# Performance work log

Measured on AMD Instinct MI355X. Metric: run time of the kernel, lower is better.

Reference implementation:

```python
import jax, jax.numpy as jnp
import numpy as np

N_NODES = 100000
N_EDGES = 500000
E_HID = 64
IN_DIM = 192  # r_hidden + 2*t_hidden
NEG_SLOPE = 0.01


def setup_inputs() -> dict:
    key = jax.random.key(0)
    ks = jax.random.split(key, 16)
    s_in = 1.0 / np.sqrt(IN_DIM)
    s_e = 1.0 / np.sqrt(E_HID)
    inp = {
        "x_e": jax.random.normal(ks[0], (N_NODES, E_HID), dtype=jnp.float32),
        "x_r": jax.random.normal(ks[1], (N_EDGES, IN_DIM), dtype=jnp.float32),
        "edge_index": jax.random.randint(ks[2], (2, N_EDGES), 0, N_NODES, dtype=jnp.int64),
        "rel_size": jnp.arange(N_EDGES, dtype=jnp.int64),
        "Wr": jax.random.uniform(ks[3], (E_HID, IN_DIM), jnp.float32, -s_in, s_in),
        "br": jax.random.uniform(ks[4], (E_HID,), jnp.float32, -s_in, s_in),
        "Wr1": jax.random.uniform(ks[5], (E_HID, IN_DIM), jnp.float32, -s_in, s_in),
        "br1": jax.random.uniform(ks[6], (E_HID,), jnp.float32, -s_in, s_in),
        "Wr2": jax.random.uniform(ks[7], (E_HID, IN_DIM), jnp.float32, -s_in, s_in),
        "br2": jax.random.uniform(ks[8], (E_HID,), jnp.float32, -s_in, s_in),
        "ah": jax.random.uniform(ks[9], (E_HID,), jnp.float32, -s_e, s_e),
        "ah1": jax.random.uniform(ks[10], (E_HID,), jnp.float32, -s_e, s_e),
        "at": jax.random.uniform(ks[11], (E_HID,), jnp.float32, -s_e, s_e),
        "ar1": jax.random.uniform(ks[12], (E_HID,), jnp.float32, -s_e, s_e),
        "ar2": jax.random.uniform(ks[13], (E_HID,), jnp.float32, -s_e, s_e),
        "ar3": jax.random.uniform(ks[14], (E_HID,), jnp.float32, -s_e, s_e),
    }
    return inp


def _gat_block(x_e, x_r, idx, rel_size, W, b, a_node, a_rel, num_nodes):
    # e_r = w_r(x_r): [E, e_hid]
    e_r = x_r @ W.T + b
    # attention logits per edge: a_node . x_e[idx] + a_rel . e_r
    logits = x_e[idx] @ a_node + e_r @ a_rel  # [E]
    lr = jnp.where(logits > 0, logits, NEG_SLOPE * logits)  # leaky_relu
    # segment softmax over destination segments (idx)
    m = jax.ops.segment_max(lr, idx, num_segments=num_nodes)
    ex = jnp.exp(lr - m[idx])
    s = jax.ops.segment_sum(ex, idx, num_segments=num_nodes)
    alpha = ex / (s[idx] + 1e-16)
    # spmm: out[n] = sum_{e: idx[e]==n} alpha[e] * e_r[rel_size[e]]
    agg = jax.ops.segment_sum(alpha[:, None] * e_r[rel_size], idx, num_segments=num_nodes)
    return x_e + jax.nn.relu(agg)


def reference(x_e, x_r, edge_index, rel_size, Wr, br, Wr1, br1, Wr2, br2,
              ah, ah1, at, ar1, ar2, ar3):
    n = x_e.shape[0]
    h, t = edge_index[0], edge_index[1]
    x_e = _gat_block(x_e, x_r, h, rel_size, Wr, br, ah, ar1, n)
    x_e = _gat_block(x_e, x_r, t, rel_size, Wr1, br1, at, ar2, n)
    x_e = _gat_block(x_e, x_r, h, rel_size, Wr2, br2, ah1, ar3, n)
    return x_e
```

## Files before the change

kernel.cpp:

```cpp
#include <hip/hip_runtime.h>
#include <hip/hip_bf16.h>

typedef __attribute__((ext_vector_type(8))) short short8;
typedef __attribute__((ext_vector_type(4))) float f32x4;

#define DEV __device__ __forceinline__

#define BARRIER() do { asm volatile("s_waitcnt lgkmcnt(0)" ::: "memory"); \
                       __builtin_amdgcn_s_barrier(); \
                       __builtin_amdgcn_sched_barrier(0); } while (0)

DEV unsigned short f2bf(float f) {
    unsigned u = __float_as_uint(f);
    u += 0x7FFFu + ((u >> 16) & 1u);
    return (unsigned short)(u >> 16);
}
DEV float bf2f(unsigned short h) { return __uint_as_float(((unsigned)h) << 16); }
DEV unsigned pk2(float lo, float hi) {
    float2 f; f.x = lo; f.y = hi;
    __hip_bfloat162 h = __float22bfloat162_rn(f);
    unsigned r; __builtin_memcpy(&r, &h, 4);
    return r;
}
union S8 { short8 s; unsigned u[4]; };

__global__ __launch_bounds__(256) void wconv_k(
    const float* __restrict__ W0, const float* __restrict__ W1,
    const float* __restrict__ W2, unsigned short* __restrict__ wbf)
{
    const int i = blockIdx.x * 256 + threadIdx.x;
    if (i >= 3 * 64 * 192) return;
    const int m = i / (64 * 192), r = i % (64 * 192);
    const float* W = (m == 0) ? W0 : ((m == 1) ? W1 : W2);
    wbf[i] = f2bf(W[r]);
}

__global__ __launch_bounds__(512, 2) void gemm_k(
    const float* __restrict__ xr, const unsigned short* __restrict__ wbf,
    const float* __restrict__ b0, const float* __restrict__ b1, const float* __restrict__ b2,
    const float* __restrict__ a0, const float* __restrict__ a1, const float* __restrict__ a2,
    unsigned short* __restrict__ er,
    float* __restrict__ ed0, float* __restrict__ ed1, float* __restrict__ ed2,
    int E, int ntiles, int K)
{
    __shared__ __align__(16) unsigned short ShBuf[192 * 192];
    unsigned short* Ws = ShBuf;
    unsigned short* As = ShBuf;
    float (*red)[64] = (float (*)[64])(ShBuf + 64 * 192);

    const int t = threadIdx.x;
    const int w = t >> 6, l = t & 63, l15 = l & 15, lg = l >> 4;
    const int cgrp = w & 3, rh = w >> 2;
    const int srow = t >> 3, sq = t & 7;

#pragma unroll
    for (int j = 0; j < 9; ++j) {
        const int c = j * 512 + t;
        const int gc = c / 24, pos = c - gc * 24;
        const short8 v = *(const short8*)(wbf + (size_t)gc * 192 + pos * 8);
        const unsigned byte = (unsigned)(gc * 384 + pos * 16);
        *(short8*)((char*)Ws + (byte ^ ((gc & 7) << 4))) = v;
    }
    BARRIER();
    short8 bfr[3][6];
#pragma unroll
    for (int i = 0; i < 3; ++i) {
        const int gc = (cgrp * 3 + i) * 16 + l15;
#pragma unroll
        for (int ks = 0; ks < 6; ++ks) {
            const unsigned byte = (unsigned)(gc * 384 + ks * 64 + lg * 16);
            bfr[i][ks] = *(const short8*)((const char*)Ws + (byte ^ ((gc & 7) << 4)));
        }
    }

    const int G = gridDim.x;
    float4 nv[6];
    if (blockIdx.x < ntiles) {
        const long e = (long)blockIdx.x * 64 + srow;
        const bool ok = e < E;
        const float* sp = xr + e * (long)K + sq * 24;
#pragma unroll
        for (int r = 0; r < 6; ++r)
            nv[r] = ok ? *(const float4*)(sp + r * 4) : make_float4(0.f, 0.f, 0.f, 0.f);
    }

    for (int tile = blockIdx.x; tile < ntiles; tile += G) {
        const long e0 = (long)tile * 64;
        BARRIER();
        {
            const unsigned swz = (unsigned)((srow & 7) << 4);
            S8 o0, o1, o2;
            o0.u[0] = pk2(nv[0].x, nv[0].y); o0.u[1] = pk2(nv[0].z, nv[0].w);
            o0.u[2] = pk2(nv[1].x, nv[1].y); o0.u[3] = pk2(nv[1].z, nv[1].w);
            o1.u[0] = pk2(nv[2].x, nv[2].y); o1.u[1] = pk2(nv[2].z, nv[2].w);
            o1.u[2] = pk2(nv[3].x, nv[3].y); o1.u[3] = pk2(nv[3].z, nv[3].w);
            o2.u[0] = pk2(nv[4].x, nv[4].y); o2.u[1] = pk2(nv[4].z, nv[4].w);
            o2.u[2] = pk2(nv[5].x, nv[5].y); o2.u[3] = pk2(nv[5].z, nv[5].w);
            const unsigned byte0 = (unsigned)(srow * 384 + sq * 48);
            *(short8*)((char*)As + ((byte0 +  0) ^ swz)) = o0.s;
            *(short8*)((char*)As + ((byte0 + 16) ^ swz)) = o1.s;
            *(short8*)((char*)As + ((byte0 + 32) ^ swz)) = o2.s;
        }
        {
            const int nxt = tile + G;
            if (nxt < ntiles) {
                const long e = (long)nxt * 64 + srow;
                const bool ok = e < E;
                const float* sp = xr + e * (long)K + sq * 24;
#pragma unroll
                for (int r = 0; r < 6; ++r)
                    nv[r] = ok ? *(const float4*)(sp + r * 4)
                               : make_float4(0.f, 0.f, 0.f, 0.f);
            }
        }
        BARRIER();
        f32x4 acc[2][3];
#pragma unroll
        for (int rt = 0; rt < 2; ++rt)
#pragma unroll
            for (int i = 0; i < 3; ++i) acc[rt][i] = (f32x4)(0.f);
#pragma unroll
        for (int ks = 0; ks < 6; ++ks) {
            short8 af[2];
#pragma unroll
            for (int rt = 0; rt < 2; ++rt) {
                const int row = rh * 32 + rt * 16 + l15;
                const unsigned byte = (unsigned)(row * 384 + ks * 64 + lg * 16);
                af[rt] = *(const short8*)((const char*)As + (byte ^ ((row & 7) << 4)));
            }
#pragma unroll
            for (int i = 0; i < 3; ++i)
#pragma unroll
                for (int rt = 0; rt < 2; ++rt)
                    acc[rt][i] = __builtin_amdgcn_mfma_f32_16x16x32_bf16(bfr[i][ks], af[rt], acc[rt][i], 0, 0, 0);
        }
#pragma unroll
        for (int i = 0; i < 3; ++i) {
            const int ct = cgrp * 3 + i, m = ct >> 2;
            const int cb_ = ((ct & 3) << 4) + (lg << 2);
            const float* bp = (m == 0) ? b0 : ((m == 1) ? b1 : b2);
            const float* ap = (m == 0) ? a0 : ((m == 1) ? a1 : a2);
            const float4 bb = *(const float4*)(bp + cb_);
            const float4 aa = *(const float4*)(ap + cb_);
            const int fb = ct * 16 + (lg << 2);
#pragma unroll
            for (int rt = 0; rt < 2; ++rt) {
                const int edge = rh * 32 + rt * 16 + l15;
                const long ee = e0 + edge;
                const float v0 = acc[rt][i][0] + bb.x;
                const float v1 = acc[rt][i][1] + bb.y;
                const float v2 = acc[rt][i][2] + bb.z;
                const float v3 = acc[rt][i][3] + bb.w;
                if (ee < E) {
                    uint2 pkv;
                    pkv.x = pk2(v0, v1);
                    pkv.y = pk2(v2, v3);
                    *(uint2*)(er + (size_t)ee * 192 + fb) = pkv;
                }
                float pd = v0 * aa.x + v1 * aa.y + v2 * aa.z + v3 * aa.w;
                pd += __shfl_xor(pd, 16);
                pd += __shfl_xor(pd, 32);
                if (lg == 0) red[ct][edge] = pd;
            }
        }
        BARRIER();
        if (t < 64) {
            const long ee = e0 + t;
            if (ee < E) {
                float s0 = 0.f, s1 = 0.f, s2 = 0.f;
#pragma unroll
                for (int q = 0; q < 4; ++q) {
                    s0 += red[q][t]; s1 += red[4 + q][t]; s2 += red[8 + q][t];
                }
                ed0[ee] = s0; ed1[ee] = s1; ed2[ee] = s2;
            }
        }
    }
}

__global__ __launch_bounds__(256) void count2_k(const int* __restrict__ h,
                                                const int* __restrict__ tt,
                                                int* __restrict__ deg, int E, int N)
{
    const int e = blockIdx.x * 256 + threadIdx.x;
    if (e >= E) return;
    atomicAdd(&deg[h[e]], 1);
    atomicAdd(&deg[N + tt[e]], 1);
}

__global__ __launch_bounds__(256) void scan1_k(const int* __restrict__ deg,
                                               int* __restrict__ incl,
                                               int* __restrict__ bsum, int M)
{
    __shared__ int buf[256];
    const int tid = threadIdx.x;
    const int n = blockIdx.x * 256 + tid;
    buf[tid] = (n < M) ? deg[n] : 0;
    __syncthreads();
    for (int d = 1; d < 256; d <<= 1) {
        int v = (tid >= d) ? buf[tid - d] : 0;
        __syncthreads();
        buf[tid] += v;
        __syncthreads();
    }
    if (n < M) incl[n] = buf[tid];
    if (tid == 255) bsum[blockIdx.x] = buf[255];
}

__global__ __launch_bounds__(256) void scan2_k(int* __restrict__ bsum, int nb)
{
    __shared__ int wsum[4];
    const int tid = threadIdx.x, l = tid & 63, wv = tid >> 6;
    int base = 0;
    for (int start = 0; start < nb; start += 1024) {
        const int i0 = start + tid * 4;
        int v0 = 0, v1 = 0, v2 = 0, v3 = 0;
        if (i0 < nb)     v0 = bsum[i0];
        if (i0 + 1 < nb) v1 = bsum[i0 + 1];
        if (i0 + 2 < nb) v2 = bsum[i0 + 2];
        if (i0 + 3 < nb) v3 = bsum[i0 + 3];
        const int tsum = v0 + v1 + v2 + v3;
        int sc = tsum;
#pragma unroll
        for (int d = 1; d < 64; d <<= 1) {
            const int o = __shfl_up(sc, d);
            if (l >= d) sc += o;
        }
        if (l == 63) wsum[wv] = sc;
        __syncthreads();
        int woff = base;
        for (int q = 0; q < wv; ++q) woff += wsum[q];
        int run = woff + sc - tsum;
        run += v0; if (i0 < nb)     bsum[i0] = run;
        run += v1; if (i0 + 1 < nb) bsum[i0 + 1] = run;
        run += v2; if (i0 + 2 < nb) bsum[i0 + 2] = run;
        run += v3; if (i0 + 3 < nb) bsum[i0 + 3] = run;
        base += wsum[0] + wsum[1] + wsum[2] + wsum[3];
        __syncthreads();
    }
}

__global__ __launch_bounds__(256) void off_k(const int* __restrict__ deg,
                                             const int* __restrict__ incl,
                                             const int* __restrict__ bsum,
                                             int* __restrict__ off,
                                             int* __restrict__ cur, int M, int tot)
{
    const int n = blockIdx.x * 256 + threadIdx.x;
    if (n < M) {
        const int prev = (blockIdx.x > 0) ? bsum[blockIdx.x - 1] : 0;
        const int o = prev + incl[n] - deg[n];
        off[n] = o;
        cur[n] = o;
    }
    if (n == 0) off[M] = tot;
}

__global__ __launch_bounds__(256) void fill2_k(const int* __restrict__ h,
                                               const int* __restrict__ tt,
                                               int* __restrict__ cur,
                                               int* __restrict__ elist, int E, int N)
{
    const int e = blockIdx.x * 256 + threadIdx.x;
    if (e >= E) return;
    const int p = atomicAdd(&cur[h[e]], 1);
    elist[p] = e;
    const int p2 = atomicAdd(&cur[N + tt[e]], 1);
    elist[p2] = e;
}

__global__ __launch_bounds__(256, 6) void gat3_k(
    const int* __restrict__ off, const int* __restrict__ elist,
    const float* __restrict__ ed0, const float* __restrict__ ed1,
    const float* __restrict__ ed2, const unsigned short* __restrict__ er,
    const float* __restrict__ xe, float* __restrict__ out,
    const float* __restrict__ an0, const float* __restrict__ an1,
    const float* __restrict__ an2, int N)
{
    __shared__ float sm[4][8][64];
    const int wv = threadIdx.x >> 6;
    const int node = blockIdx.x * 4 + wv;
    if (node >= N) return;
    const int l = threadIdx.x & 63;
    const int g = l >> 3, q = l & 7;

    const int h0 = off[node], h1 = off[node + 1];
    const int t0 = off[N + node], t1 = off[N + node + 1];
    float x = xe[(size_t)node * 64 + l];

    if ((h1 - h0) <= 8 && (t1 - t0) <= 8) {
        const bool vh = g < (h1 - h0), vt = g < (t1 - t0);
        const int eh = vh ? elist[h0 + g] : 0;
        const int et = vt ? elist[t0 + g] : 0;
        const float edv0 = vh ? ed0[eh] : 0.f;
        const float edv1 = vt ? ed1[et] : 0.f;
        const float edv2 = vh ? ed2[eh] : 0.f;
        short8 w0, w1, w2;
        w0 = vh ? *(const short8*)(er + (size_t)eh * 192 +       q * 8) : (short8)(short)0;
        w1 = vt ? *(const short8*)(er + (size_t)et * 192 +  64 + q * 8) : (short8)(short)0;
        w2 = vh ? *(const short8*)(er + (size_t)eh * 192 + 128 + q * 8) : (short8)(short)0;

#pragma unroll
        for (int b = 0; b < 3; ++b) {
            const float* anb = (b == 0) ? an0 : ((b == 1) ? an1 : an2);
            const bool val = (b == 1) ? vt : vh;
            const float edv = (b == 0) ? edv0 : ((b == 1) ? edv1 : edv2);
            const short8 vv = (b == 0) ? w0 : ((b == 1) ? w1 : w2);

            float pv = x * anb[l];
#pragma unroll
            for (int d = 1; d < 64; d <<= 1) pv += __shfl_xor(pv, d);

            const float lr = pv + edv;
            const float lv = lr > 0.f ? lr : 0.01f * lr;
            float mt = val ? lv : -1e30f;
            mt = fmaxf(mt, __shfl_xor(mt, 8));
            mt = fmaxf(mt, __shfl_xor(mt, 16));
            mt = fmaxf(mt, __shfl_xor(mt, 32));
            const float wg = val ? __expf(lv - mt) : 0.f;
            float s = wg;
            s += __shfl_xor(s, 8);
            s += __shfl_xor(s, 16);
            s += __shfl_xor(s, 32);

            f32x4 aA, aB;
            aA[0] = wg * bf2f((unsigned short)vv[0]);
            aA[1] = wg * bf2f((unsigned short)vv[1]);
            aA[2] = wg * bf2f((unsigned short)vv[2]);
            aA[3] = wg * bf2f((unsigned short)vv[3]);
            aB[0] = wg * bf2f((unsigned short)vv[4]);
            aB[1] = wg * bf2f((unsigned short)vv[5]);
            aB[2] = wg * bf2f((unsigned short)vv[6]);
            aB[3] = wg * bf2f((unsigned short)vv[7]);
            *(f32x4*)&sm[wv][g][q * 8] = aA;
            *(f32x4*)&sm[wv][g][q * 8 + 4] = aB;
            asm volatile("s_waitcnt lgkmcnt(0)" ::: "memory");
            __builtin_amdgcn_sched_barrier(0);
            float a = 0.f;
#pragma unroll
            for (int gg = 0; gg < 8; ++gg) a += sm[wv][gg][l];
            asm volatile("s_waitcnt lgkmcnt(0)" ::: "memory");
            __builtin_amdgcn_sched_barrier(0);

            x += fmaxf(a / (s + 1e-16f), 0.f);
        }
    } else {
#pragma unroll
        for (int b = 0; b < 3; ++b) {
            const float* edb = (b == 0) ? ed0 : ((b == 1) ? ed1 : ed2);
            const float* anb = (b == 0) ? an0 : ((b == 1) ? an1 : an2);
            const int cb = b * 64;
            const int s0 = (b == 1) ? t0 : h0, s1 = (b == 1) ? t1 : h1;

            float pv = x * anb[l];
#pragma unroll
            for (int d = 1; d < 64; d <<= 1) pv += __shfl_xor(pv, d);

            float m = -1e30f, s = 0.f;
            f32x4 aA = (f32x4)(0.f), aB = (f32x4)(0.f);
            for (int j = s0; j < s1; j += 8) {
                const int jj = j + g;
                if (jj < s1) {
                    const int e = elist[jj];
                    const float lg_ = pv + edb[e];
                    const float lv = lg_ > 0.f ? lg_ : 0.01f * lg_;
                    const short8 v = *(const short8*)(er + (size_t)e * 192 + cb + q * 8);
                    const float nm = fmaxf(m, lv);
                    const float rs = __expf(m - nm);
                    const float wg = __expf(lv - nm);
                    s = s * rs + wg;
                    aA[0] = aA[0] * rs + wg * bf2f((unsigned short)v[0]);
                    aA[1] = aA[1] * rs + wg * bf2f((unsigned short)v[1]);
                    aA[2] = aA[2] * rs + wg * bf2f((unsigned short)v[2]);
                    aA[3] = aA[3] * rs + wg * bf2f((unsigned short)v[3]);
                    aB[0] = aB[0] * rs + wg * bf2f((unsigned short)v[4]);
                    aB[1] = aB[1] * rs + wg * bf2f((unsigned short)v[5]);
                    aB[2] = aB[2] * rs + wg * bf2f((unsigned short)v[6]);
                    aB[3] = aB[3] * rs + wg * bf2f((unsigned short)v[7]);
                    m = nm;
                }
            }
            float mt = m;
            mt = fmaxf(mt, __shfl_xor(mt, 8));
            mt = fmaxf(mt, __shfl_xor(mt, 16));
            mt = fmaxf(mt, __shfl_xor(mt, 32));
            const float rs2 = __expf(m - mt);
            s *= rs2;
            s += __shfl_xor(s, 8);
            s += __shfl_xor(s, 16);
            s += __shfl_xor(s, 32);
#pragma unroll
            for (int c = 0; c < 4; ++c) { aA[c] *= rs2; aB[c] *= rs2; }
            *(f32x4*)&sm[wv][g][q * 8] = aA;
            *(f32x4*)&sm[wv][g][q * 8 + 4] = aB;
            asm volatile("s_waitcnt lgkmcnt(0)" ::: "memory");
            __builtin_amdgcn_sched_barrier(0);
            float a = 0.f;
#pragma unroll
            for (int gg = 0; gg < 8; ++gg) a += sm[wv][gg][l];
            asm volatile("s_waitcnt lgkmcnt(0)" ::: "memory");
            __builtin_amdgcn_sched_barrier(0);

            x += fmaxf(a / (s + 1e-16f), 0.f);
        }
    }
    out[(size_t)node * 64 + l] = x;
}

extern "C" void kernel_launch(void* const* d_in, const int* in_sizes, int n_in,
                              void* d_out, int out_size, void* d_ws, size_t ws_size,
                              hipStream_t stream)
{
    const float* xe  = (const float*)d_in[0];
    const float* xr  = (const float*)d_in[1];
    const int*   eix = (const int*)d_in[2];
    const float* Wr  = (const float*)d_in[4];
    const float* br  = (const float*)d_in[5];
    const float* Wr1 = (const float*)d_in[6];
    const float* br1 = (const float*)d_in[7];
    const float* Wr2 = (const float*)d_in[8];
    const float* br2 = (const float*)d_in[9];
    const float* ah  = (const float*)d_in[10];
    const float* ah1 = (const float*)d_in[11];
    const float* at_ = (const float*)d_in[12];
    const float* ar1 = (const float*)d_in[13];
    const float* ar2 = (const float*)d_in[14];
    const float* ar3 = (const float*)d_in[15];

    const int E = in_sizes[3];
    const int N = in_sizes[0] / 64;
    const int K = in_sizes[1] / E;
    const int M = 2 * N;
    float* out = (float*)d_out;

    char* p = (char*)d_ws;
    auto carve = [&](size_t bytes) -> void* {
        void* r = (void*)p;
        p += (bytes + 255) & ~(size_t)255;
        return r;
    };
    const int nb = (M + 255) / 256;
    unsigned short* er = (unsigned short*)carve((size_t)(E + 64) * 192 * 2);
    float* ed0 = (float*)carve((size_t)(E + 64) * 4);
    float* ed1 = (float*)carve((size_t)(E + 64) * 4);
    float* ed2 = (float*)carve((size_t)(E + 64) * 4);
    unsigned short* wbf = (unsigned short*)carve((size_t)3 * 64 * 192 * 2);
    int* off = (int*)carve((size_t)(M + 1) * 4);
    int* elist = (int*)carve((size_t)2 * E * 4);
    int* deg = (int*)carve((size_t)M * 4);
    int* incl = (int*)carve((size_t)M * 4);
    int* cur = (int*)carve((size_t)M * 4);
    int* bsum = (int*)carve((size_t)nb * 4);
    (void)ws_size;

    const int Eg = (E + 255) / 256;
    const int ng = (N + 3) / 4;
    const int ntiles = (E + 63) / 64;
    const int ggrid = ntiles < 512 ? ntiles : 512;

    wconv_k<<<(3 * 64 * 192 + 255) / 256, 256, 0, stream>>>(Wr, Wr1, Wr2, wbf);

    hipMemsetAsync(deg, 0, (size_t)M * 4, stream);
    count2_k<<<Eg, 256, 0, stream>>>(eix, eix + E, deg, E, N);
    scan1_k<<<nb, 256, 0, stream>>>(deg, incl, bsum, M);
    scan2_k<<<1, 256, 0, stream>>>(bsum, nb);
    off_k<<<nb, 256, 0, stream>>>(deg, incl, bsum, off, cur, M, 2 * E);
    fill2_k<<<Eg, 256, 0, stream>>>(eix, eix + E, cur, elist, E, N);

    gemm_k<<<ggrid, 512, 0, stream>>>(xr, wbf, br, br1, br2, ar1, ar2, ar3,
                                      er, ed0, ed1, ed2, E, ntiles, K);

    gat3_k<<<ng, 256, 0, stream>>>(off, elist, ed0, ed1, ed2, er, xe, out,
                                   ah, at_, ah1, N);
}
```

Before: 370.4 us.

## Compute edge attention dot in GAT kernel and double-buffer GEMM LDS tile

The GEMM kernel no longer computes or stores the per-edge dot products of e_r with the ar vectors. The GAT kernel now recomputes them from the bf16 e_r row it already loads, using a shuffle reduction across the 8 lanes that share an edge. The GEMM A tile is also double-buffered in LDS, which removes one barrier per tile and the reduction barrier. This saves the ed writes and the scattered ed reads, but adds a shuffle reduction to every edge step of the online-softmax loop, and the logits now come from bf16-rounded e_r.

```diff
diff --git a/kernel.cpp b/kernel.cpp
--- a/kernel.cpp
+++ b/kernel.cpp
@@ -38,16 +38,11 @@
 __global__ __launch_bounds__(512, 2) void gemm_k(
     const float* __restrict__ xr, const unsigned short* __restrict__ wbf,
     const float* __restrict__ b0, const float* __restrict__ b1, const float* __restrict__ b2,
-    const float* __restrict__ a0, const float* __restrict__ a1, const float* __restrict__ a2,
     unsigned short* __restrict__ er,
-    float* __restrict__ ed0, float* __restrict__ ed1, float* __restrict__ ed2,
     int E, int ntiles, int K)
 {
     __shared__ __align__(16) unsigned short ShBuf[192 * 192];
     unsigned short* Ws = ShBuf;
-    unsigned short* As = ShBuf;
-    float (*red)[64] = (float (*)[64])(ShBuf + 64 * 192);
-
     const int t = threadIdx.x;
     const int w = t >> 6, l = t & 63, l15 = l & 15, lg = l >> 4;
     const int cgrp = w & 3, rh = w >> 2;
@@ -61,17 +56,6 @@
         const unsigned byte = (unsigned)(gc * 384 + pos * 16);
         *(short8*)((char*)Ws + (byte ^ ((gc & 7) << 4))) = v;
     }
-    BARRIER();
-    short8 bfr[3][6];
-#pragma unroll
-    for (int i = 0; i < 3; ++i) {
-        const int gc = (cgrp * 3 + i) * 16 + l15;
-#pragma unroll
-        for (int ks = 0; ks < 6; ++ks) {
-            const unsigned byte = (unsigned)(gc * 384 + ks * 64 + lg * 16);
-            bfr[i][ks] = *(const short8*)((const char*)Ws + (byte ^ ((gc & 7) << 4)));
-        }
-    }
 
     const int G = gridDim.x;
     float4 nv[6];
@@ -84,9 +68,23 @@
             nv[r] = ok ? *(const float4*)(sp + r * 4) : make_float4(0.f, 0.f, 0.f, 0.f);
     }
 
-    for (int tile = blockIdx.x; tile < ntiles; tile += G) {
+    BARRIER();
+    short8 bfr[3][6];
+#pragma unroll
+    for (int i = 0; i < 3; ++i) {
+        const int gc = (cgrp * 3 + i) * 16 + l15;
+#pragma unroll
+        for (int ks = 0; ks < 6; ++ks) {
+            const unsigned byte = (unsigned)(gc * 384 + ks * 64 + lg * 16);
+            bfr[i][ks] = *(const short8*)((const char*)Ws + (byte ^ ((gc & 7) << 4)));
+        }
+    }
+    BARRIER();
+
+    int p = 0;
+    for (int tile = blockIdx.x; tile < ntiles; tile += G, p ^= 1) {
         const long e0 = (long)tile * 64;
-        BARRIER();
+        char* Ab = (char*)(ShBuf + p * 64 * 192);
         {
             const unsigned swz = (unsigned)((srow & 7) << 4);
             S8 o0, o1, o2;
@@ -97,9 +95,9 @@
             o2.u[0] = pk2(nv[4].x, nv[4].y); o2.u[1] = pk2(nv[4].z, nv[4].w);
             o2.u[2] = pk2(nv[5].x, nv[5].y); o2.u[3] = pk2(nv[5].z, nv[5].w);
             const unsigned byte0 = (unsigned)(srow * 384 + sq * 48);
-            *(short8*)((char*)As + ((byte0 +  0) ^ swz)) = o0.s;
-            *(short8*)((char*)As + ((byte0 + 16) ^ swz)) = o1.s;
-            *(short8*)((char*)As + ((byte0 + 32) ^ swz)) = o2.s;
+            *(short8*)(Ab + ((byte0 +  0) ^ swz)) = o0.s;
+            *(short8*)(Ab + ((byte0 + 16) ^ swz)) = o1.s;
+            *(short8*)(Ab + ((byte0 + 32) ^ swz)) = o2.s;
         }
         {
             const int nxt = tile + G;
@@ -126,7 +124,7 @@
             for (int rt = 0; rt < 2; ++rt) {
                 const int row = rh * 32 + rt * 16 + l15;
                 const unsigned byte = (unsigned)(row * 384 + ks * 64 + lg * 16);
-                af[rt] = *(const short8*)((const char*)As + (byte ^ ((row & 7) << 4)));
+                af[rt] = *(const short8*)((const char*)Ab + (byte ^ ((row & 7) << 4)));
             }
 #pragma unroll
             for (int i = 0; i < 3; ++i)
@@ -139,40 +137,18 @@
             const int ct = cgrp * 3 + i, m = ct >> 2;
             const int cb_ = ((ct & 3) << 4) + (lg << 2);
             const float* bp = (m == 0) ? b0 : ((m == 1) ? b1 : b2);
-            const float* ap = (m == 0) ? a0 : ((m == 1) ? a1 : a2);
             const float4 bb = *(const float4*)(bp + cb_);
-            const float4 aa = *(const float4*)(ap + cb_);
             const int fb = ct * 16 + (lg << 2);
 #pragma unroll
             for (int rt = 0; rt < 2; ++rt) {
                 const int edge = rh * 32 + rt * 16 + l15;
                 const long ee = e0 + edge;
-                const float v0 = acc[rt][i][0] + bb.x;
-                const float v1 = acc[rt][i][1] + bb.y;
-                const float v2 = acc[rt][i][2] + bb.z;
-                const float v3 = acc[rt][i][3] + bb.w;
                 if (ee < E) {
                     uint2 pkv;
-                    pkv.x = pk2(v0, v1);
-                    pkv.y = pk2(v2, v3);
+                    pkv.x = pk2(acc[rt][i][0] + bb.x, acc[rt][i][1] + bb.y);
+                    pkv.y = pk2(acc[rt][i][2] + bb.z, acc[rt][i][3] + bb.w);
                     *(uint2*)(er + (size_t)ee * 192 + fb) = pkv;
                 }
-                float pd = v0 * aa.x + v1 * aa.y + v2 * aa.z + v3 * aa.w;
-                pd += __shfl_xor(pd, 16);
-                pd += __shfl_xor(pd, 32);
-                if (lg == 0) red[ct][edge] = pd;
-            }
-        }
-        BARRIER();
-        if (t < 64) {
-            const long ee = e0 + t;
-            if (ee < E) {
-                float s0 = 0.f, s1 = 0.f, s2 = 0.f;
-#pragma unroll
-                for (int q = 0; q < 4; ++q) {
-                    s0 += red[q][t]; s1 += red[4 + q][t]; s2 += red[8 + q][t];
-                }
-                ed0[ee] = s0; ed1[ee] = s1; ed2[ee] = s2;
             }
         }
     }
@@ -271,11 +247,12 @@
 
 __global__ __launch_bounds__(256, 6) void gat3_k(
     const int* __restrict__ off, const int* __restrict__ elist,
-    const float* __restrict__ ed0, const float* __restrict__ ed1,
-    const float* __restrict__ ed2, const unsigned short* __restrict__ er,
+    const unsigned short* __restrict__ er,
     const float* __restrict__ xe, float* __restrict__ out,
     const float* __restrict__ an0, const float* __restrict__ an1,
-    const float* __restrict__ an2, int N)
+    const float* __restrict__ an2,
+    const float* __restrict__ ar0, const float* __restrict__ ar1,
+    const float* __restrict__ ar2, int N)
 {
     __shared__ float sm[4][8][64];
     const int wv = threadIdx.x >> 6;
@@ -292,9 +269,6 @@
         const bool vh = g < (h1 - h0), vt = g < (t1 - t0);
         const int eh = vh ? elist[h0 + g] : 0;
         const int et = vt ? elist[t0 + g] : 0;
-        const float edv0 = vh ? ed0[eh] : 0.f;
-        const float edv1 = vt ? ed1[et] : 0.f;
-        const float edv2 = vh ? ed2[eh] : 0.f;
         short8 w0, w1, w2;
         w0 = vh ? *(const short8*)(er + (size_t)eh * 192 +       q * 8) : (short8)(short)0;
         w1 = vt ? *(const short8*)(er + (size_t)et * 192 +  64 + q * 8) : (short8)(short)0;
@@ -303,15 +277,29 @@
 #pragma unroll
         for (int b = 0; b < 3; ++b) {
             const float* anb = (b == 0) ? an0 : ((b == 1) ? an1 : an2);
+            const float* arb = (b == 0) ? ar0 : ((b == 1) ? ar1 : ar2);
             const bool val = (b == 1) ? vt : vh;
-            const float edv = (b == 0) ? edv0 : ((b == 1) ? edv1 : edv2);
             const short8 vv = (b == 0) ? w0 : ((b == 1) ? w1 : w2);
 
             float pv = x * anb[l];
 #pragma unroll
             for (int d = 1; d < 64; d <<= 1) pv += __shfl_xor(pv, d);
 
-            const float lr = pv + edv;
+            const float4 a1 = *(const float4*)(arb + q * 8);
+            const float4 a2 = *(const float4*)(arb + q * 8 + 4);
+            float dd = bf2f((unsigned short)vv[0]) * a1.x
+                     + bf2f((unsigned short)vv[1]) * a1.y
+                     + bf2f((unsigned short)vv[2]) * a1.z
+                     + bf2f((unsigned short)vv[3]) * a1.w
+                     + bf2f((unsigned short)vv[4]) * a2.x
+                     + bf2f((unsigned short)vv[5]) * a2.y
+                     + bf2f((unsigned short)vv[6]) * a2.z
+                     + bf2f((unsigned short)vv[7]) * a2.w;
+            dd += __shfl_xor(dd, 1);
+            dd += __shfl_xor(dd, 2);
+            dd += __shfl_xor(dd, 4);
+
+            const float lr = pv + dd;
             const float lv = lr > 0.f ? lr : 0.01f * lr;
             float mt = val ? lv : -1e30f;
             mt = fmaxf(mt, __shfl_xor(mt, 8));
@@ -347,14 +335,16 @@
     } else {
 #pragma unroll
         for (int b = 0; b < 3; ++b) {
-            const float* edb = (b == 0) ? ed0 : ((b == 1) ? ed1 : ed2);
             const float* anb = (b == 0) ? an0 : ((b == 1) ? an1 : an2);
+            const float* arb = (b == 0) ? ar0 : ((b == 1) ? ar1 : ar2);
             const int cb = b * 64;
             const int s0 = (b == 1) ? t0 : h0, s1 = (b == 1) ? t1 : h1;
 
             float pv = x * anb[l];
 #pragma unroll
             for (int d = 1; d < 64; d <<= 1) pv += __shfl_xor(pv, d);
+            const float4 a1 = *(const float4*)(arb + q * 8);
+            const float4 a2 = *(const float4*)(arb + q * 8 + 4);
 
             float m = -1e30f, s = 0.f;
             f32x4 aA = (f32x4)(0.f), aB = (f32x4)(0.f);
@@ -362,9 +352,20 @@
                 const int jj = j + g;
                 if (jj < s1) {
                     const int e = elist[jj];
-                    const float lg_ = pv + edb[e];
+                    const short8 v = *(const short8*)(er + (size_t)e * 192 + cb + q * 8);
+                    float dd = bf2f((unsigned short)v[0]) * a1.x
+                             + bf2f((unsigned short)v[1]) * a1.y
+                             + bf2f((unsigned short)v[2]) * a1.z
+                             + bf2f((unsigned short)v[3]) * a1.w
+                             + bf2f((unsigned short)v[4]) * a2.x
+                             + bf2f((unsigned short)v[5]) * a2.y
+                             + bf2f((unsigned short)v[6]) * a2.z
+                             + bf2f((unsigned short)v[7]) * a2.w;
+                    dd += __shfl_xor(dd, 1);
+                    dd += __shfl_xor(dd, 2);
+                    dd += __shfl_xor(dd, 4);
+                    const float lg_ = pv + dd;
                     const float lv = lg_ > 0.f ? lg_ : 0.01f * lg_;
-                    const short8 v = *(const short8*)(er + (size_t)e * 192 + cb + q * 8);
                     const float nm = fmaxf(m, lv);
                     const float rs = __expf(m - nm);
                     const float wg = __expf(lv - nm);
@@ -441,9 +442,6 @@
     };
     const int nb = (M + 255) / 256;
     unsigned short* er = (unsigned short*)carve((size_t)(E + 64) * 192 * 2);
-    float* ed0 = (float*)carve((size_t)(E + 64) * 4);
-    float* ed1 = (float*)carve((size_t)(E + 64) * 4);
-    float* ed2 = (float*)carve((size_t)(E + 64) * 4);
     unsigned short* wbf = (unsigned short*)carve((size_t)3 * 64 * 192 * 2);
     int* off = (int*)carve((size_t)(M + 1) * 4);
     int* elist = (int*)carve((size_t)2 * E * 4);
@@ -467,9 +465,8 @@
     off_k<<<nb, 256, 0, stream>>>(deg, incl, bsum, off, cur, M, 2 * E);
     fill2_k<<<Eg, 256, 0, stream>>>(eix, eix + E, cur, elist, E, N);
 
-    gemm_k<<<ggrid, 512, 0, stream>>>(xr, wbf, br, br1, br2, ar1, ar2, ar3,
-                                      er, ed0, ed1, ed2, E, ntiles, K);
-
-    gat3_k<<<ng, 256, 0, stream>>>(off, elist, ed0, ed1, ed2, er, xe, out,
-                                   ah, at_, ah1, N);
-}
+    gemm_k<<<ggrid, 512, 0, stream>>>(xr, wbf, br, br1, br2, er, E, ntiles, K);
+
+    gat3_k<<<ng, 256, 0, stream>>>(off, elist, er, xe, out,
+                                   ah, at_, ah1, ar1, ar2, ar3, N);
+}
```

New measurement: 357.5 us. 1.04x faster.
